# Optimization experiments

Measured on AMD Instinct MI355X. Metric: run time of the kernel, lower is better.

Reference implementation:

```python
import jax, jax.numpy as jnp
import numpy as np
from jax import lax

EPS = 1e-20  # matches sample_gumbel eps in the TF source


def setup_inputs() -> dict:
    key = jax.random.key(0)
    ks = jax.random.split(key, 7)
    B, T, D, H, K = 32, 512, 512, 512, 64
    x = jax.random.normal(ks[0], (B, T, D), jnp.float32)
    f_after = jax.random.normal(ks[1], (K, D, H), jnp.float32) * 0.02
    f_skip = jax.random.normal(ks[2], (2 * H, 2), jnp.float32) * 0.05
    gru_kernel = jax.random.normal(ks[3], (D, 3 * H), jnp.float32) * 0.02
    gru_rec_kernel = jax.random.normal(ks[4], (H, 3 * H), jnp.float32) * 0.02
    gru_bias = jnp.zeros((2, 3 * H), jnp.float32)
    u_gumbel = jax.random.uniform(ks[5], (T, B, 2), jnp.float32)
    return {"x": x, "f_after": f_after, "f_skip": f_skip,
            "gru_kernel": gru_kernel, "gru_rec_kernel": gru_rec_kernel,
            "gru_bias": gru_bias, "u_gumbel": u_gumbel}


def reference(x, f_after, f_skip, gru_kernel, gru_rec_kernel, gru_bias, u_gumbel):
    # z_after = tanh(conv1d(x, f_after, SAME))  -> [B, T, H]
    z_after = lax.conv_general_dilated(
        x, f_after, window_strides=(1,), padding='SAME',
        dimension_numbers=('NWC', 'WIO', 'NWC'))
    z_after = jnp.tanh(z_after)

    # gumbel(0,1) noise from uniform draws, per step: [T, B, 2]
    g = -jnp.log(-jnp.log(u_gumbel + EPS) + EPS)

    b_in, b_rec = gru_bias[0], gru_bias[1]  # reset_after=True biases, each [3H]
    H = gru_rec_kernel.shape[0]
    B = x.shape[0]
    h0 = jnp.zeros((B, H), x.dtype)

    xs = (jnp.swapaxes(x, 0, 1), jnp.swapaxes(z_after, 0, 1), g)  # time-major

    def step(h_prev, inp):
        x_t, za_t, g_t = inp
        # skip gate: concat(h_{t-1}, z_after_t) @ f_skip, gumbel-softmax (temp=1)
        logits = jnp.concatenate([h_prev, za_t], axis=-1) @ f_skip  # [B, 2]
        skip = jax.nn.softmax(logits + g_t, axis=-1)
        # Keras GRUCell (reset_after=True), gate order z, r, h
        xm = x_t @ gru_kernel + b_in          # [B, 3H]
        hm = h_prev @ gru_rec_kernel + b_rec  # [B, 3H]
        xz, xr, xh = jnp.split(xm, 3, axis=-1)
        hz, hr, hh = jnp.split(hm, 3, axis=-1)
        z = jax.nn.sigmoid(xz + hz)
        r = jax.nn.sigmoid(xr + hr)
        hc = jnp.tanh(xh + r * hh)
        ht = z * h_prev + (1.0 - z) * hc
        # skip blend
        ht = skip[:, 0:1] * h_prev + skip[:, 1:2] * ht
        return ht, ht

    _, ys = lax.scan(step, h0, xs)           # [T, B, H]
    return jnp.swapaxes(ys, 0, 1)            # [B, T, H]
```

## Files before the change

kernel.cpp:

```cpp
#include <hip/hip_runtime.h>
#include <stdint.h>

typedef unsigned short u16;
typedef unsigned int   u32;
typedef __attribute__((ext_vector_type(8))) short short8;
typedef __attribute__((ext_vector_type(4))) float f32x4;
typedef __attribute__((ext_vector_type(4))) u32   u32x4;

#define AS1 __attribute__((address_space(1)))
#define AS3 __attribute__((address_space(3)))

#define SENT 0x7FC0u
#define HS   528

__device__ __forceinline__ float bf2f(u16 u) {
  union { u32 i; float f; } v; v.i = ((u32)u) << 16; return v.f;
}
__device__ __forceinline__ u16 f2bf(float f) {
  union { float f; u32 i; } v; v.f = f;
  u32 i = v.i;
  i += 0x7FFFu + ((i >> 16) & 1u);
  return (u16)(i >> 16);
}
__device__ __forceinline__ float tanh_fast(float x) {
  const float e = __expf(-2.f * fabsf(x));
  const float t = (1.f - e) / (1.f + e);
  return __builtin_copysignf(t, x);
}

__device__ __forceinline__ void gload16(const u16* src, u16* ldsDst) {
  __builtin_amdgcn_global_load_lds((const AS1 u32*)src, (AS3 u32*)ldsDst, 16, 0, 0);
}

__device__ __forceinline__ short8 ldg_sc_h_wait(const u16* p) {
  short8 r;
  asm volatile("global_load_dwordx4 %0, %1, off sc0 sc1\n\t"
               "s_waitcnt vmcnt(0)"
               : "=v"(r) : "v"(p) : "memory");
  return r;
}
__device__ __forceinline__ void stg_sc_h(u16* p, u16 v) {
  asm volatile("global_store_short %0, %1, off sc0 sc1" :: "v"(p), "v"((u32)v) : "memory");
}

__global__ void k_init(const float* __restrict__ x, u16* __restrict__ xp) {
  const long NXP = 32L * 576 * 512;
  long i0 = (long)blockIdx.x * 256 + threadIdx.x;
  for (long i = i0; i < NXP; i += (long)gridDim.x * 256) {
    long b = i / (576 * 512);
    int rem = (int)(i - b * (576 * 512));
    int rr = rem >> 9, dd = rem & 511;
    int t = rr - 31;
    float v = (t >= 0 && t < 512) ? x[(b * 512 + t) * 512 + dd] : 0.f;
    xp[i] = f2bf(v);
  }
}

__global__ void k_sent(u32* __restrict__ hs) {
  const u32x4 s = u32x4{(SENT << 16) | SENT, (SENT << 16) | SENT,
                        (SENT << 16) | SENT, (SENT << 16) | SENT};
  *(u32x4*)&hs[((long)blockIdx.x * 256 + threadIdx.x) * 4] = s;
}

__global__ void k_transpose_cast(const float* __restrict__ in, u16* __restrict__ out,
                                 int rows, int cols, long inWStride, long outWStride) {
  __shared__ float tile[64][65];
  const int w = blockIdx.z;
  const float* ip = in + (long)w * inWStride;
  u16* op = out + (long)w * outWStride;
  const int r0 = blockIdx.y * 64, c0 = blockIdx.x * 64;
  const int tr = threadIdx.x >> 6, tc = threadIdx.x & 63;
  #pragma unroll
  for (int p = 0; p < 16; ++p) {
    int rr = p * 4 + tr;
    tile[rr][tc] = ip[(long)(r0 + rr) * cols + c0 + tc];
  }
  __syncthreads();
  #pragma unroll
  for (int p = 0; p < 16; ++p) {
    int rr = p * 4 + tr;
    op[(long)(c0 + rr) * rows + r0 + tc] = f2bf(tile[tc][rr]);
  }
}

__global__ __launch_bounds__(256) void k_gemm(
    const u16* __restrict__ A, const u16* __restrict__ Bm, u16* __restrict__ C,
    int nTiles, int kw, int woff, long bWStride, int outMode)
{
  __shared__ __align__(16) u16 Alds[128 * 64];
  __shared__ __align__(16) u16 Blds[128 * 64];
  const int bid0 = blockIdx.x;
  const int cpx = gridDim.x >> 3;
  const int bid = (bid0 & 7) * cpx + (bid0 >> 3);
  const int mt = bid / nTiles, nt = bid - mt * nTiles;
  const int bb = (mt * 128) >> 9;
  const int t0 = (mt * 128) & 511;
  const int h0 = nt * 128;
  const int tid = threadIdx.x;
  const int wv = tid >> 6, l = tid & 63;
  const int wr = wv >> 1, wc = wv & 1;
  const int sRow = wv * 8 + (l >> 3);
  const int sCol = (l & 7) * 8;
  f32x4 acc[4][4];
  #pragma unroll
  for (int m = 0; m < 4; ++m)
    #pragma unroll
    for (int n = 0; n < 4; ++n) acc[m][n] = f32x4{0.f, 0.f, 0.f, 0.f};

  const int kIters = kw * 8;
  const long aRow0 = (long)(bb * 576 + t0 + woff);
  for (int q = 0; q < kIters; ++q) {
    const int w = q >> 3, dsub = (q & 7) << 6;
    const u16* aB = A + (aRow0 + w) * 512 + dsub + sCol;
    const u16* bB = Bm + (long)w * bWStride + (long)h0 * 512 + dsub + sCol;
    __syncthreads();
    #pragma unroll
    for (int c = 0; c < 4; ++c) {
      gload16(aB + (long)(c * 32 + sRow) * 512, &Alds[c * 2048 + wv * 512]);
      gload16(bB + (long)(c * 32 + sRow) * 512, &Blds[c * 2048 + wv * 512]);
    }
    __syncthreads();
    #pragma unroll
    for (int kk = 0; kk < 2; ++kk) {
      short8 af[4], bf[4];
      #pragma unroll
      for (int m = 0; m < 4; ++m)
        af[m] = *(const short8*)&Alds[(wr * 64 + m * 16 + (l & 15)) * 64 + kk * 32 + (l >> 4) * 8];
      #pragma unroll
      for (int n = 0; n < 4; ++n)
        bf[n] = *(const short8*)&Blds[(wc * 64 + n * 16 + (l & 15)) * 64 + kk * 32 + (l >> 4) * 8];
      #pragma unroll
      for (int m = 0; m < 4; ++m)
        #pragma unroll
        for (int n = 0; n < 4; ++n)
          acc[m][n] = __builtin_amdgcn_mfma_f32_16x16x32_bf16(af[m], bf[n], acc[m][n], 0, 0, 0);
    }
  }
  const int lr = (l >> 4) * 4, lc = l & 15;
  #pragma unroll
  for (int m = 0; m < 4; ++m)
    #pragma unroll
    for (int n = 0; n < 4; ++n)
      #pragma unroll
      for (int r = 0; r < 4; ++r) {
        const int row = mt * 128 + wr * 64 + m * 16 + lr + r;
        const int col = h0 + wc * 64 + n * 16 + lc;
        const float v = acc[m][n][r];
        if (outMode == 0) {
          C[(long)row * 512 + col] = f2bf(tanhf(v));
        } else {
          const int b = row >> 9, t = row & 511;
          C[((long)t * 32 + b) * 1536 + col] = f2bf(v);
        }
      }
}

__global__ void k_dza(const u16* __restrict__ za, const float* __restrict__ fskip,
                      const float* __restrict__ ug, float* __restrict__ dza) {
  __shared__ float wd2[512];
  const int t = blockIdx.x, tid = threadIdx.x;
  for (int i = tid; i < 512; i += 256) wd2[i] = fskip[(512 + i) * 2 + 1] - fskip[(512 + i) * 2];
  __syncthreads();
  const int b = tid >> 3, seg = (tid & 7) * 64;
  const u16* row = za + ((long)b * 512 + t) * 512 + seg;
  float pp = 0.f;
  #pragma unroll
  for (int j = 0; j < 8; ++j) {
    short8 v = *(const short8*)&row[j * 8];
    #pragma unroll
    for (int e = 0; e < 8; ++e) pp += bf2f((u16)v[e]) * wd2[seg + j * 8 + e];
  }
  pp += __shfl_xor(pp, 1); pp += __shfl_xor(pp, 2); pp += __shfl_xor(pp, 4);
  if ((tid & 7) == 0) {
    float u0 = ug[((long)t * 32 + b) * 2 + 0], u1 = ug[((long)t * 32 + b) * 2 + 1];
    float g0 = -logf(-logf(u0 + 1e-20f) + 1e-20f);
    float g1 = -logf(-logf(u1 + 1e-20f) + 1e-20f);
    dza[t * 32 + b] = pp + (g1 - g0);
  }
}

__global__ __launch_bounds__(256, 1) void k_rnn(
    const u16* __restrict__ XM, const float* __restrict__ dza,
    const float* __restrict__ Wrec, const float* __restrict__ gbias,
    const float* __restrict__ fskip, u16* hstep, float* __restrict__ out)
{
  const int bid = blockIdx.x, d = bid & 7, s = bid >> 3;
  const int tid = threadIdx.x, wv = tid >> 6, l = tid & 63;
  __shared__ __align__(16) u16 hBl[2][4 * HS];
  __shared__ float s1s[2][4];

  float wdv[8];
  #pragma unroll
  for (int e = 0; e < 8; ++e)
    wdv[e] = fskip[(l * 8 + e) * 2 + 1] - fskip[(l * 8 + e) * 2];

  const int colb = s * 64 + wv * 16 + (l & 15);
  const int kq = (l >> 4) * 8;

  short8 wf[3][16];
  #pragma unroll
  for (int g = 0; g < 3; ++g)
    #pragma unroll
    for (int kk = 0; kk < 16; ++kk) {
      short8 tmp;
      #pragma unroll
      for (int e = 0; e < 8; ++e)
        tmp[e] = (short)f2bf(Wrec[(long)(kk * 32 + kq + e) * 1536 + g * 512 + colb]);
      wf[g][kk] = tmp;
    }
  float bi[3], br[3];
  #pragma unroll
  for (int g = 0; g < 3; ++g) {
    bi[g] = gbias[g * 512 + colb];
    br[g] = gbias[1536 + g * 512 + colb];
  }
  const int myb = d * 4;
  float hp[4] = {0.f, 0.f, 0.f, 0.f};
  float hnv[4] = {0.f, 0.f, 0.f, 0.f};

  u16 xmc[3][4];
  float dzc;
  if (l < 16) {
    const u16* xr = XM + (long)myb * 1536;
    #pragma unroll
    for (int r = 0; r < 4; ++r)
      #pragma unroll
      for (int g = 0; g < 3; ++g)
        xmc[g][r] = xr[(long)r * 1536 + g * 512 + colb];
  }
  dzc = dza[myb + wv];

  for (int t = 0; t < 512; ++t) {
    const int p = t & 1;

    short8 h8;
    if (t > 0) {
      const u16* ph = hstep + ((long)(t - 1) * 32 + myb + wv) * 512 + l * 8;
      h8 = ldg_sc_h_wait(ph);
      bool bad = true;
      while (bad) {
        bad = false;
        #pragma unroll
        for (int e = 0; e < 8; ++e) bad |= ((u16)h8[e] == SENT);
        if (bad) h8 = ldg_sc_h_wait(ph);
      }
    } else {
      #pragma unroll
      for (int e = 0; e < 8; ++e) h8[e] = 0;
    }

    if (t > 0 && l < 16) {
      #pragma unroll
      for (int r = 0; r < 4; ++r)
        out[((long)(myb + r) * 512 + (t - 1)) * 512 + colb] = hnv[r];
    }

    u16 xmn[3][4];
    const int tn = (t < 511) ? t + 1 : t;
    if (l < 16) {
      const u16* xr = XM + ((long)tn * 32 + myb) * 1536;
      #pragma unroll
      for (int r = 0; r < 4; ++r)
        #pragma unroll
        for (int g = 0; g < 3; ++g)
          xmn[g][r] = xr[(long)r * 1536 + g * 512 + colb];
    }
    const float dzn = dza[tn * 32 + myb + wv];

    *(short8*)&hBl[p][wv * HS + l * 8] = h8;
    float pp = 0.f;
    #pragma unroll
    for (int e = 0; e < 8; ++e) pp += bf2f((u16)h8[e]) * wdv[e];
    #pragma unroll
    for (int o = 1; o < 64; o <<= 1) pp += __shfl_xor(pp, o);
    if (l == 0) s1s[p][wv] = 1.f / (1.f + __expf(-(pp + dzc)));
    __syncthreads();

    f32x4 acc[3];
    acc[0] = f32x4{0.f, 0.f, 0.f, 0.f}; acc[1] = acc[0]; acc[2] = acc[0];
    const int b4 = l & 3;
    #pragma unroll
    for (int kk = 0; kk < 16; ++kk) {
      short8 a = *(const short8*)&hBl[p][b4 * HS + kk * 32 + kq];
      acc[0] = __builtin_amdgcn_mfma_f32_16x16x32_bf16(a, wf[0][kk], acc[0], 0, 0, 0);
      acc[1] = __builtin_amdgcn_mfma_f32_16x16x32_bf16(a, wf[1][kk], acc[1], 0, 0, 0);
      acc[2] = __builtin_amdgcn_mfma_f32_16x16x32_bf16(a, wf[2][kk], acc[2], 0, 0, 0);
    }

    if (l < 16) {
      #pragma unroll
      for (int r = 0; r < 4; ++r) {
        const float xz = bf2f(xmc[0][r]) + bi[0];
        const float xr_ = bf2f(xmc[1][r]) + bi[1];
        const float xh = bf2f(xmc[2][r]) + bi[2];
        const float hz = acc[0][r] + br[0];
        const float hr = acc[1][r] + br[1];
        const float hh = acc[2][r] + br[2];
        const float z  = 1.f / (1.f + __expf(-(xz + hz)));
        const float rr = 1.f / (1.f + __expf(-(xr_ + hr)));
        const float hc = tanh_fast(xh + rr * hh);
        const float ht = z * hp[r] + (1.f - z) * hc;
        const float s1 = s1s[p][r];
        const float hn = hp[r] + s1 * (ht - hp[r]);
        stg_sc_h(&hstep[((long)t * 32 + myb + r) * 512 + colb], f2bf(hn));
        hp[r] = hn;
        hnv[r] = hn;
      }
      #pragma unroll
      for (int g = 0; g < 3; ++g)
        #pragma unroll
        for (int r = 0; r < 4; ++r) xmc[g][r] = xmn[g][r];
    }
    dzc = dzn;
  }
  if (l < 16) {
    #pragma unroll
    for (int r = 0; r < 4; ++r)
      out[((long)(myb + r) * 512 + 511) * 512 + colb] = hnv[r];
  }
}

extern "C" void kernel_launch(void* const* d_in, const int* in_sizes, int n_in,
                              void* d_out, int out_size, void* d_ws, size_t ws_size,
                              hipStream_t stream) {
  (void)in_sizes; (void)n_in; (void)out_size; (void)ws_size;
  const float* x        = (const float*)d_in[0];
  const float* f_after  = (const float*)d_in[1];
  const float* f_skip   = (const float*)d_in[2];
  const float* gru_k    = (const float*)d_in[3];
  const float* gru_rec  = (const float*)d_in[4];
  const float* gru_bias = (const float*)d_in[5];
  const float* ug       = (const float*)d_in[6];
  float* out = (float*)d_out;

  char* ws = (char*)d_ws;
  size_t off = 0;
  auto alloc = [&](size_t bytes) { void* p = ws + off; off = (off + bytes + 255) & ~(size_t)255; return p; };
  u16*  xp    = (u16*)alloc(32L * 576 * 512 * 2);
  u16*  fT    = (u16*)alloc(64L * 512 * 512 * 2);
  u16*  gruT  = (u16*)alloc(1536L * 512 * 2);
  u16*  za    = (u16*)alloc(32L * 512 * 512 * 2);
  u16*  XM    = (u16*)alloc(512L * 32 * 1536 * 2);
  float* dza  = (float*)alloc(512L * 32 * 4);
  u16*  hstep = za;

  k_init<<<dim3(4096), dim3(256), 0, stream>>>(x, xp);
  k_transpose_cast<<<dim3(8, 8, 64), dim3(256), 0, stream>>>(f_after, fT, 512, 512, 512L * 512, 512L * 512);
  k_transpose_cast<<<dim3(24, 8, 1), dim3(256), 0, stream>>>(gru_k, gruT, 512, 1536, 0L, 0L);
  k_gemm<<<dim3(512), dim3(256), 0, stream>>>(xp, fT, za, 4, 64, 0, 512L * 512, 0);
  k_gemm<<<dim3(1536), dim3(256), 0, stream>>>(xp, gruT, XM, 12, 1, 31, 0L, 1);
  k_dza<<<dim3(512), dim3(256), 0, stream>>>(za, f_skip, ug, dza);
  k_sent<<<dim3(4096), dim3(256), 0, stream>>>((u32*)hstep);
  k_rnn<<<dim3(64), dim3(256), 0, stream>>>(XM, dza, gru_rec, gru_bias, f_skip, hstep, out);
}
```

Baseline: 2.111 ms.

## Pin RNN blocks per XCD via atomic slots and poll L2 copy first

The recurrent kernel now launches many blocks and keeps only eight per XCD, chosen by an atomic slot counter keyed on the hardware XCC id. Each group of blocks working on the same batch slice therefore shares one XCD's L2. Each step's hidden state is written twice: once with L2-coherent stores and once with system-coherent stores. Consumers poll the L2 copy first for a bounded number of tries and then fall back to the memory copy, to cut cross-block handoff latency. This relies on the hardware scheduler placing at least eight blocks on every XCD and on those blocks being co-resident. It adds an extra sentinel fill and doubles the hidden-state stores.

```diff
diff --git a/kernel.cpp b/kernel.cpp
--- a/kernel.cpp
+++ b/kernel.cpp
@@ -42,8 +42,19 @@
 __device__ __forceinline__ void stg_sc_h(u16* p, u16 v) {
   asm volatile("global_store_short %0, %1, off sc0 sc1" :: "v"(p), "v"((u32)v) : "memory");
 }
-
-__global__ void k_init(const float* __restrict__ x, u16* __restrict__ xp) {
+__device__ __forceinline__ short8 ldg_l2_wait(const u16* p) {
+  short8 r;
+  asm volatile("global_load_dwordx4 %0, %1, off sc0\n\t"
+               "s_waitcnt vmcnt(0)"
+               : "=v"(r) : "v"(p) : "memory");
+  return r;
+}
+__device__ __forceinline__ void stg_l2(u16* p, u16 v) {
+  asm volatile("global_store_short %0, %1, off sc0" :: "v"(p), "v"((u32)v) : "memory");
+}
+
+__global__ void k_init(const float* __restrict__ x, u16* __restrict__ xp,
+                       u32* __restrict__ xcdslot) {
   const long NXP = 32L * 576 * 512;
   long i0 = (long)blockIdx.x * 256 + threadIdx.x;
   for (long i = i0; i < NXP; i += (long)gridDim.x * 256) {
@@ -54,6 +65,7 @@
     float v = (t >= 0 && t < 512) ? x[(b * 512 + t) * 512 + dd] : 0.f;
     xp[i] = f2bf(v);
   }
+  if (i0 < 8) xcdslot[i0] = 0u;
 }
 
 __global__ void k_sent(u32* __restrict__ hs) {
@@ -182,12 +194,24 @@
 __global__ __launch_bounds__(256, 1) void k_rnn(
     const u16* __restrict__ XM, const float* __restrict__ dza,
     const float* __restrict__ Wrec, const float* __restrict__ gbias,
-    const float* __restrict__ fskip, u16* hstep, float* __restrict__ out)
+    const float* __restrict__ fskip, u16* hL2, u16* hM,
+    float* __restrict__ out, u32* __restrict__ xcdslot)
 {
-  const int bid = blockIdx.x, d = bid & 7, s = bid >> 3;
   const int tid = threadIdx.x, wv = tid >> 6, l = tid & 63;
   __shared__ __align__(16) u16 hBl[2][4 * HS];
   __shared__ float s1s[2][4];
+  __shared__ u32 slotS;
+
+  u32 xcc;
+  asm volatile("s_getreg_b32 %0, hwreg(HW_REG_XCC_ID)" : "=s"(xcc));
+  xcc &= 7u;
+  if (tid == 0)
+    slotS = __hip_atomic_fetch_add(&xcdslot[xcc], 1u, __ATOMIC_RELAXED,
+                                   __HIP_MEMORY_SCOPE_AGENT);
+  __syncthreads();
+  const u32 slot = slotS;
+  if (slot >= 8u) return;
+  const int d = (int)xcc, s = (int)slot;
 
   float wdv[8];
   #pragma unroll
@@ -235,14 +259,21 @@
 
     short8 h8;
     if (t > 0) {
-      const u16* ph = hstep + ((long)(t - 1) * 32 + myb + wv) * 512 + l * 8;
-      h8 = ldg_sc_h_wait(ph);
+      const long hoff = ((long)(t - 1) * 32 + myb + wv) * 512 + l * 8;
       bool bad = true;
+      #pragma unroll 1
+      for (int it = 0; it < 10 && bad; ++it) {
+        h8 = ldg_l2_wait(hL2 + hoff);
+        bad = false;
+        #pragma unroll
+        for (int e = 0; e < 8; ++e) bad |= ((u16)h8[e] == SENT);
+      }
+      #pragma unroll 1
       while (bad) {
+        h8 = ldg_sc_h_wait(hM + hoff);
         bad = false;
         #pragma unroll
         for (int e = 0; e < 8; ++e) bad |= ((u16)h8[e] == SENT);
-        if (bad) h8 = ldg_sc_h_wait(ph);
       }
     } else {
       #pragma unroll
@@ -302,7 +333,10 @@
         const float ht = z * hp[r] + (1.f - z) * hc;
         const float s1 = s1s[p][r];
         const float hn = hp[r] + s1 * (ht - hp[r]);
-        stg_sc_h(&hstep[((long)t * 32 + myb + r) * 512 + colb], f2bf(hn));
+        const u16 hb = f2bf(hn);
+        const long go = ((long)t * 32 + myb + r) * 512 + colb;
+        stg_l2(&hL2[go], hb);
+        stg_sc_h(&hM[go], hb);
         hp[r] = hn;
         hnv[r] = hn;
       }
@@ -342,14 +376,17 @@
   u16*  za    = (u16*)alloc(32L * 512 * 512 * 2);
   u16*  XM    = (u16*)alloc(512L * 32 * 1536 * 2);
   float* dza  = (float*)alloc(512L * 32 * 4);
-  u16*  hstep = za;
-
-  k_init<<<dim3(4096), dim3(256), 0, stream>>>(x, xp);
+  u32*  slot  = (u32*)alloc(64);
+  u16*  hL2   = za;
+  u16*  hM    = fT;
+
+  k_init<<<dim3(4096), dim3(256), 0, stream>>>(x, xp, slot);
   k_transpose_cast<<<dim3(8, 8, 64), dim3(256), 0, stream>>>(f_after, fT, 512, 512, 512L * 512, 512L * 512);
   k_transpose_cast<<<dim3(24, 8, 1), dim3(256), 0, stream>>>(gru_k, gruT, 512, 1536, 0L, 0L);
   k_gemm<<<dim3(512), dim3(256), 0, stream>>>(xp, fT, za, 4, 64, 0, 512L * 512, 0);
   k_gemm<<<dim3(1536), dim3(256), 0, stream>>>(xp, gruT, XM, 12, 1, 31, 0L, 1);
   k_dza<<<dim3(512), dim3(256), 0, stream>>>(za, f_skip, ug, dza);
-  k_sent<<<dim3(4096), dim3(256), 0, stream>>>((u32*)hstep);
-  k_rnn<<<dim3(64), dim3(256), 0, stream>>>(XM, dza, gru_rec, gru_bias, f_skip, hstep, out);
-}
+  k_sent<<<dim3(4096), dim3(256), 0, stream>>>((u32*)hL2);
+  k_sent<<<dim3(4096), dim3(256), 0, stream>>>((u32*)hM);
+  k_rnn<<<dim3(2048), dim3(256), 0, stream>>>(XM, dza, gru_rec, gru_bias, f_skip, hL2, hM, out, slot);
+}
```

Result: slower. 2.170 ms (+2.8%).

## Add dedicated conv kernel reusing a sliding A window across filter taps

Applied to the files above, without the earlier changes.

Replaces the generic GEMM launch for the conv with a specialized kernel. It loads a 192-row slab of the padded input into LDS once per 64-wide input-channel chunk and reuses it for all 64 filter taps by offsetting the row index. Only the per-tap weight tile is reloaded each iteration, which cuts global A traffic by about a factor of 64. The inner loop loads synchronously with two barriers per tap and no double buffering, so latency may be exposed, and the A-fragment reads at shifted row offsets may cause LDS bank conflicts.

```diff
diff --git a/kernel.cpp b/kernel.cpp
--- a/kernel.cpp
+++ b/kernel.cpp
@@ -81,6 +81,74 @@
     int rr = p * 4 + tr;
     op[(long)(c0 + rr) * rows + r0 + tc] = f2bf(tile[tc][rr]);
   }
+}
+
+__global__ __launch_bounds__(256) void k_conv(
+    const u16* __restrict__ A, const u16* __restrict__ Bm, u16* __restrict__ C)
+{
+  __shared__ __align__(16) u16 Abig[192 * 64];
+  __shared__ __align__(16) u16 Blds[128 * 64];
+  const int bid0 = blockIdx.x;
+  const int bid = (bid0 & 7) * 64 + (bid0 >> 3);
+  const int mt = bid & 127, nt = bid >> 7;
+  const int bb = (mt * 128) >> 9;
+  const int t0 = (mt * 128) & 511;
+  const int h0 = nt * 128;
+  const int tid = threadIdx.x;
+  const int wv = tid >> 6, l = tid & 63;
+  const int wr = wv >> 1, wc = wv & 1;
+  const int sRow = wv * 8 + (l >> 3);
+  const int sCol = (l & 7) * 8;
+  f32x4 acc[4][4];
+  #pragma unroll
+  for (int m = 0; m < 4; ++m)
+    #pragma unroll
+    for (int n = 0; n < 4; ++n) acc[m][n] = f32x4{0.f, 0.f, 0.f, 0.f};
+
+  const long aRow0 = (long)(bb * 576 + t0);
+  for (int dsub = 0; dsub < 8; ++dsub) {
+    const int dcol = dsub << 6;
+    for (int w = 0; w < 64; ++w) {
+      __syncthreads();
+      if (w == 0) {
+        #pragma unroll
+        for (int c = 0; c < 6; ++c)
+          gload16(A + (aRow0 + c * 32 + sRow) * 512 + dcol + sCol,
+                  &Abig[(c * 32 + wv * 8) * 64]);
+      }
+      #pragma unroll
+      for (int c = 0; c < 4; ++c)
+        gload16(Bm + ((long)w << 18) + (long)(h0 + c * 32 + sRow) * 512 + dcol + sCol,
+                &Blds[(c * 32 + wv * 8) * 64]);
+      __syncthreads();
+      #pragma unroll
+      for (int kk = 0; kk < 2; ++kk) {
+        short8 af[4], bf[4];
+        #pragma unroll
+        for (int m = 0; m < 4; ++m)
+          af[m] = *(const short8*)&Abig[(w + wr * 64 + m * 16 + (l & 15)) * 64 + kk * 32 + (l >> 4) * 8];
+        #pragma unroll
+        for (int n = 0; n < 4; ++n)
+          bf[n] = *(const short8*)&Blds[(wc * 64 + n * 16 + (l & 15)) * 64 + kk * 32 + (l >> 4) * 8];
+        #pragma unroll
+        for (int m = 0; m < 4; ++m)
+          #pragma unroll
+          for (int n = 0; n < 4; ++n)
+            acc[m][n] = __builtin_amdgcn_mfma_f32_16x16x32_bf16(af[m], bf[n], acc[m][n], 0, 0, 0);
+      }
+    }
+  }
+  const int lr = (l >> 4) * 4, lc = l & 15;
+  #pragma unroll
+  for (int m = 0; m < 4; ++m)
+    #pragma unroll
+    for (int n = 0; n < 4; ++n)
+      #pragma unroll
+      for (int r = 0; r < 4; ++r) {
+        const int row = mt * 128 + wr * 64 + m * 16 + lr + r;
+        const int col = h0 + wc * 64 + n * 16 + lc;
+        C[(long)row * 512 + col] = f2bf(tanhf(acc[m][n][r]));
+      }
 }
 
 __global__ __launch_bounds__(256) void k_gemm(
@@ -347,7 +415,7 @@
   k_init<<<dim3(4096), dim3(256), 0, stream>>>(x, xp);
   k_transpose_cast<<<dim3(8, 8, 64), dim3(256), 0, stream>>>(f_after, fT, 512, 512, 512L * 512, 512L * 512);
   k_transpose_cast<<<dim3(24, 8, 1), dim3(256), 0, stream>>>(gru_k, gruT, 512, 1536, 0L, 0L);
-  k_gemm<<<dim3(512), dim3(256), 0, stream>>>(xp, fT, za, 4, 64, 0, 512L * 512, 0);
+  k_conv<<<dim3(512), dim3(256), 0, stream>>>(xp, fT, za);
   k_gemm<<<dim3(1536), dim3(256), 0, stream>>>(xp, gruT, XM, 12, 1, 31, 0L, 1);
   k_dza<<<dim3(512), dim3(256), 0, stream>>>(za, f_skip, ug, dza);
   k_sent<<<dim3(4096), dim3(256), 0, stream>>>((u32*)hstep);
```

Measured after the change: 2.009 ms. 4.8% less time.
